# Optimization experiments

Hardware: AMD Instinct MI355X
Metric: run time of the kernel (lower is better)

Reference implementation:

```python
import jax, jax.numpy as jnp
import numpy as np

D_MODEL = 1024
NUM_HEADS = 16
HEAD_DIM = D_MODEL // NUM_HEADS


def setup_inputs() -> dict:
    key = jax.random.key(0)
    ks = jax.random.split(key, 5)
    x = jax.random.normal(ks[0], (2, 2048, D_MODEL), dtype=jnp.float32)
    # torch.nn.Linear default init ~ U(-1/sqrt(fan_in), 1/sqrt(fan_in)); scale roughly
    s = 1.0 / np.sqrt(D_MODEL)
    W_qkv = jax.random.uniform(ks[1], (D_MODEL, 3 * D_MODEL), jnp.float32, -s, s)
    b_qkv = jax.random.uniform(ks[2], (3 * D_MODEL,), jnp.float32, -s, s)
    W_out = jax.random.uniform(ks[3], (D_MODEL, D_MODEL), jnp.float32, -s, s)
    b_out = jax.random.uniform(ks[4], (D_MODEL,), jnp.float32, -s, s)
    return {"x": x, "W_qkv": W_qkv, "b_qkv": b_qkv, "W_out": W_out, "b_out": b_out}


def reference(x, W_qkv, b_qkv, W_out, b_out):
    B, S, D = x.shape
    H, Hd = NUM_HEADS, HEAD_DIM
    qkv = x @ W_qkv + b_qkv                      # [B,S,3D]
    q, k, v = jnp.split(qkv, 3, axis=-1)
    def split_heads(t):
        return t.reshape(B, S, H, Hd).transpose(0, 2, 1, 3)  # [B,H,S,Hd]
    q, k, v = split_heads(q), split_heads(k), split_heads(v)
    scores = jnp.einsum('bhqd,bhkd->bhqk', q, k) / jnp.sqrt(jnp.float32(Hd))
    weights = jax.nn.softmax(scores, axis=-1)
    attn = jnp.einsum('bhqk,bhkd->bhqd', weights, v)
    attn = attn.transpose(0, 2, 1, 3).reshape(B, S, D)
    return attn @ W_out + b_out
```

## Files before the change

kernel.cpp:

```cpp
#include <hip/hip_runtime.h>
#include <hip/hip_bf16.h>

#define DMODEL 1024
#define NH 16
#define HD 64
#define SEQ 2048
#define BATCH 2
#define BH (BATCH * NH)
#define MTOT (BATCH * SEQ)

typedef _Float16 f16x8 __attribute__((ext_vector_type(8)));
typedef _Float16 f16x4 __attribute__((ext_vector_type(4)));
typedef _Float16 f16x2 __attribute__((ext_vector_type(2)));
typedef float f32x4 __attribute__((ext_vector_type(4)));
typedef float f32x16 __attribute__((ext_vector_type(16)));

__device__ __forceinline__ void gload_lds16(const void* g, void* l) {
  __builtin_amdgcn_global_load_lds((const __attribute__((address_space(1))) unsigned*)g,
                                   (__attribute__((address_space(3))) unsigned*)l, 16, 0, 0);
}

__global__ __launch_bounds__(256) void cvt_f2h(const float* __restrict__ in,
                                               _Float16* __restrict__ out, int n8) {
  const int i = blockIdx.x * 256 + threadIdx.x;
  if (i < n8) {
    const float4 a = ((const float4*)in)[i * 2];
    const float4 b = ((const float4*)in)[i * 2 + 1];
    f16x8 o = {(_Float16)a.x, (_Float16)a.y, (_Float16)a.z, (_Float16)a.w,
               (_Float16)b.x, (_Float16)b.y, (_Float16)b.z, (_Float16)b.w};
    *(f16x8*)&out[(size_t)i * 8] = o;
  }
}

__global__ __launch_bounds__(256) void cvt_transpose(const float* __restrict__ W,
                                                     _Float16* __restrict__ Wt,
                                                     int N, int K) {
  __shared__ float Ls[64][65];
  const int k0 = blockIdx.y * 64, n0 = blockIdx.x * 64;
  const int t = threadIdx.x;
  const int r = t >> 2, c4 = (t & 3) * 16;
#pragma unroll
  for (int j = 0; j < 4; ++j) {
    const float4 v = *(const float4*)&W[(size_t)(k0 + r) * N + n0 + c4 + j * 4];
    Ls[r][c4 + j * 4 + 0] = v.x;
    Ls[r][c4 + j * 4 + 1] = v.y;
    Ls[r][c4 + j * 4 + 2] = v.z;
    Ls[r][c4 + j * 4 + 3] = v.w;
  }
  __syncthreads();
  f16x8 o0, o1;
#pragma unroll
  for (int j = 0; j < 8; ++j) {
    o0[j] = (_Float16)Ls[c4 + j][r];
    o1[j] = (_Float16)Ls[c4 + 8 + j][r];
  }
  *(f16x8*)&Wt[(size_t)(n0 + r) * K + k0 + c4] = o0;
  *(f16x8*)&Wt[(size_t)(n0 + r) * K + k0 + c4 + 8] = o1;
}

__global__ __launch_bounds__(256) void qkv_mm(const _Float16* __restrict__ A,
                                              const _Float16* __restrict__ Bt,
                                              const float* __restrict__ bias,
                                              _Float16* __restrict__ qh,
                                              _Float16* __restrict__ kh,
                                              _Float16* __restrict__ vh) {
  __shared__ __align__(16) _Float16 As[128 * 64];
  __shared__ __align__(16) _Float16 Bs[128 * 64];
  const int t = threadIdx.x;
  const int w = t >> 6, lane = t & 63;
  const int g = lane >> 4, lr = lane & 15;
  const int m0 = blockIdx.y * 128, n0 = blockIdx.x * 128;
  const int wr = w >> 1, wc = w & 1;
  const int srow = (lane >> 3);
  const int col8 = (lane & 7) * 8;
  f32x4 acc[4][4] = {};

  for (int k0 = 0; k0 < DMODEL; k0 += 64) {
    __syncthreads();
#pragma unroll
    for (int i = 0; i < 4; ++i) {
      const int row = w * 32 + i * 8 + srow;
      gload_lds16(A + (size_t)(m0 + row) * DMODEL + k0 + col8, &As[(w * 4 + i) * 512]);
      gload_lds16(Bt + (size_t)(n0 + row) * DMODEL + k0 + col8, &Bs[(w * 4 + i) * 512]);
    }
    __syncthreads();
#pragma unroll
    for (int ks = 0; ks < 2; ++ks) {
      f16x8 af[4], bf[4];
#pragma unroll
      for (int mi = 0; mi < 4; ++mi)
        af[mi] = *(const f16x8*)&As[(wr * 64 + mi * 16 + lr) * 64 + ks * 32 + g * 8];
#pragma unroll
      for (int ni = 0; ni < 4; ++ni)
        bf[ni] = *(const f16x8*)&Bs[(wc * 64 + ni * 16 + lr) * 64 + ks * 32 + g * 8];
#pragma unroll
      for (int mi = 0; mi < 4; ++mi)
#pragma unroll
        for (int ni = 0; ni < 4; ++ni)
          acc[mi][ni] = __builtin_amdgcn_mfma_f32_16x16x32_f16(af[mi], bf[ni], acc[mi][ni], 0, 0, 0);
    }
  }

#pragma unroll
  for (int ni = 0; ni < 4; ++ni) {
    const int n = n0 + wc * 64 + ni * 16 + lr;
    const float bn = bias[n];
    const int which = n >> 10, d = n & 1023, h = d >> 6, hd = d & 63;
    _Float16* dst = which == 0 ? qh : which == 1 ? kh : vh;
    const float scale = which == 0 ? 0.18033688011f : 1.0f;
#pragma unroll
    for (int mi = 0; mi < 4; ++mi)
#pragma unroll
      for (int r = 0; r < 4; ++r) {
        const int m = m0 + wr * 64 + mi * 16 + g * 4 + r;
        const int bb = m >> 11, ss = m & 2047;
        dst[((size_t)(bb * NH + h) * SEQ + ss) * HD + hd] =
            (_Float16)((acc[mi][ni][r] + bn) * scale);
      }
  }
}

__global__ __launch_bounds__(256, 2) void attn_fused(const _Float16* __restrict__ qh,
                                                     const _Float16* __restrict__ kh,
                                                     const _Float16* __restrict__ vh,
                                                     _Float16* __restrict__ ao) {
  __shared__ __align__(16) _Float16 Vt[64][76];
  const int t = threadIdx.x;
  const int lane = t & 63, w = t >> 6;
  const int q = lane & 31, hi = lane >> 5;
  const int wgid = blockIdx.x;
  const int bh = (wgid & 7) * 4 + ((wgid >> 3) & 3);
  const int qt = wgid >> 5;
  const int q0 = qt * 128 + w * 32;
  const _Float16* Qp = qh + (size_t)bh * SEQ * HD;
  const _Float16* Kp = kh + (size_t)bh * SEQ * HD;
  const _Float16* Vp = vh + (size_t)bh * SEQ * HD;

  f16x8 qf[4];
#pragma unroll
  for (int ks = 0; ks < 4; ++ks)
    qf[ks] = *(const f16x8*)(Qp + (size_t)(q0 + q) * HD + ks * 16 + hi * 8);

  f32x16 o0 = {}, o1 = {};
  float mrun = -3e30f, lrun = 0.f;

  const int skv = t & 63;
  const int sq4 = t >> 6;

  for (int kv0 = 0; kv0 < SEQ; kv0 += 64) {
    const f16x8 sv0 = *(const f16x8*)(Vp + (size_t)(kv0 + skv) * HD + sq4 * 16);
    const f16x8 sv1 = *(const f16x8*)(Vp + (size_t)(kv0 + skv) * HD + sq4 * 16 + 8);
    __syncthreads();
#pragma unroll
    for (int e = 0; e < 8; ++e) {
      Vt[sq4 * 16 + e][skv] = sv0[e];
      Vt[sq4 * 16 + 8 + e][skv] = sv1[e];
    }

    f32x16 s0 = {}, s1 = {};
    __builtin_amdgcn_s_setprio(1);
#pragma unroll
    for (int ks = 0; ks < 4; ++ks) {
      const f16x8 k0 = *(const f16x8*)(Kp + (size_t)(kv0 + q) * HD + ks * 16 + hi * 8);
      const f16x8 k1 = *(const f16x8*)(Kp + (size_t)(kv0 + 32 + q) * HD + ks * 16 + hi * 8);
      s0 = __builtin_amdgcn_mfma_f32_32x32x16_f16(k0, qf[ks], s0, 0, 0, 0);
      s1 = __builtin_amdgcn_mfma_f32_32x32x16_f16(k1, qf[ks], s1, 0, 0, 0);
    }
    __builtin_amdgcn_s_setprio(0);

    float tm[16];
#pragma unroll
    for (int r = 0; r < 16; ++r) tm[r] = fmaxf(s0[r], s1[r]);
#pragma unroll
    for (int d = 8; d > 0; d >>= 1)
#pragma unroll
      for (int r = 0; r < d; ++r) tm[r] = fmaxf(tm[r], tm[r + d]);
    const float mx = fmaxf(tm[0], __shfl_xor(tm[0], 32));
    if (!__all(mx <= mrun + 8.0f)) {
      const float mnew = fmaxf(mrun, mx);
      const float corr = exp2f(mrun - mnew);
      mrun = mnew;
      lrun *= corr;
#pragma unroll
      for (int r = 0; r < 16; ++r) {
        o0[r] *= corr;
        o1[r] *= corr;
      }
    }
#pragma unroll
    for (int r = 0; r < 16; ++r) {
      s0[r] = exp2f(s0[r] - mrun);
      s1[r] = exp2f(s1[r] - mrun);
    }
    float ts[16];
#pragma unroll
    for (int r = 0; r < 16; ++r) ts[r] = s0[r] + s1[r];
#pragma unroll
    for (int d = 8; d > 0; d >>= 1)
#pragma unroll
      for (int r = 0; r < d; ++r) ts[r] += ts[r + d];
    lrun += ts[0] + __shfl_xor(ts[0], 32);

    __syncthreads();

#pragma unroll
    for (int ks = 0; ks < 4; ++ks) {
      const int base = 8 * (ks & 1);
      unsigned u0, u1, u2, u3;
#pragma unroll
      for (int w01 = 0; w01 < 2; ++w01) {
        float a0, a1, b0, b1;
        if (ks < 2) {
          a0 = s0[base + 2 * w01];     a1 = s0[base + 2 * w01 + 1];
          b0 = s0[base + 4 + 2 * w01]; b1 = s0[base + 4 + 2 * w01 + 1];
        } else {
          a0 = s1[base + 2 * w01];     a1 = s1[base + 2 * w01 + 1];
          b0 = s1[base + 4 + 2 * w01]; b1 = s1[base + 4 + 2 * w01 + 1];
        }
        f16x2 hm0; hm0[0] = (_Float16)a0; hm0[1] = (_Float16)a1;
        f16x2 hm1; hm1[0] = (_Float16)b0; hm1[1] = (_Float16)b1;
        unsigned Pm0, Pm1;
        __builtin_memcpy(&Pm0, &hm0, 4);
        __builtin_memcpy(&Pm1, &hm1, 4);
        const unsigned local = hi ? Pm1 : Pm0;
        const unsigned sent = hi ? Pm0 : Pm1;
        const unsigned cross = __shfl_xor(sent, 32);
        const unsigned wa = hi ? cross : local;
        const unsigned wb = hi ? local : cross;
        if (w01 == 0) { u0 = wa; u2 = wb; } else { u1 = wa; u3 = wb; }
      }
      unsigned ww[4] = {u0, u1, u2, u3};
      f16x8 pb;
      __builtin_memcpy(&pb, ww, 16);
      const f16x8 va0 = *(const f16x8*)&Vt[0 + q][ks * 16 + hi * 8];
      const f16x8 va1 = *(const f16x8*)&Vt[32 + q][ks * 16 + hi * 8];
      __builtin_amdgcn_s_setprio(1);
      o0 = __builtin_amdgcn_mfma_f32_32x32x16_f16(va0, pb, o0, 0, 0, 0);
      o1 = __builtin_amdgcn_mfma_f32_32x32x16_f16(va1, pb, o1, 0, 0, 0);
      __builtin_amdgcn_s_setprio(0);
    }
  }

  const float invl = 1.0f / lrun;
  _Float16* aob = ao + (size_t)bh * SEQ * HD + (size_t)(q0 + q) * HD;
#pragma unroll
  for (int m = 0; m < 4; ++m) {
    f16x4 v0, v1;
#pragma unroll
    for (int s2 = 0; s2 < 4; ++s2) {
      v0[s2] = (_Float16)(o0[4 * m + s2] * invl);
      v1[s2] = (_Float16)(o1[4 * m + s2] * invl);
    }
    *(f16x4*)(aob + 8 * m + 4 * hi) = v0;
    *(f16x4*)(aob + 32 + 8 * m + 4 * hi) = v1;
  }
}

__global__ __launch_bounds__(256) void out_mm(const _Float16* __restrict__ Ah,
                                              const _Float16* __restrict__ Bt,
                                              const float* __restrict__ bias,
                                              float* __restrict__ out) {
  __shared__ __align__(16) _Float16 As[128 * 64];
  __shared__ __align__(16) _Float16 Bs[128 * 64];
  const int t = threadIdx.x;
  const int w = t >> 6, lane = t & 63;
  const int g = lane >> 4, lr = lane & 15;
  const int m0 = blockIdx.y * 128, n0 = blockIdx.x * 128;
  const int wr = w >> 1, wc = w & 1;
  const int srow = (lane >> 3);
  const int col8 = (lane & 7) * 8;
  f32x4 acc[4][4] = {};

  for (int k0 = 0; k0 < DMODEL; k0 += 64) {
    const int h = k0 >> 6;
    __syncthreads();
#pragma unroll
    for (int i = 0; i < 4; ++i) {
      const int row = w * 32 + i * 8 + srow;
      const int m = m0 + row;
      const int bb = m >> 11, ss = m & 2047;
      gload_lds16(Ah + ((size_t)(bb * NH + h) * SEQ + ss) * HD + col8, &As[(w * 4 + i) * 512]);
      gload_lds16(Bt + (size_t)(n0 + row) * DMODEL + k0 + col8, &Bs[(w * 4 + i) * 512]);
    }
    __syncthreads();
#pragma unroll
    for (int ks = 0; ks < 2; ++ks) {
      f16x8 af[4], bf[4];
#pragma unroll
      for (int mi = 0; mi < 4; ++mi)
        af[mi] = *(const f16x8*)&As[(wr * 64 + mi * 16 + lr) * 64 + ks * 32 + g * 8];
#pragma unroll
      for (int ni = 0; ni < 4; ++ni)
        bf[ni] = *(const f16x8*)&Bs[(wc * 64 + ni * 16 + lr) * 64 + ks * 32 + g * 8];
#pragma unroll
      for (int mi = 0; mi < 4; ++mi)
#pragma unroll
        for (int ni = 0; ni < 4; ++ni)
          acc[mi][ni] = __builtin_amdgcn_mfma_f32_16x16x32_f16(af[mi], bf[ni], acc[mi][ni], 0, 0, 0);
    }
  }

#pragma unroll
  for (int ni = 0; ni < 4; ++ni) {
    const int n = n0 + wc * 64 + ni * 16 + lr;
    const float bn = bias[n];
#pragma unroll
    for (int mi = 0; mi < 4; ++mi)
#pragma unroll
      for (int r = 0; r < 4; ++r) {
        const int m = m0 + wr * 64 + mi * 16 + g * 4 + r;
        out[(size_t)m * DMODEL + n] = acc[mi][ni][r] + bn;
      }
  }
}

extern "C" void kernel_launch(void* const* d_in, const int* in_sizes, int n_in,
                              void* d_out, int out_size, void* d_ws, size_t ws_size,
                              hipStream_t stream) {
  const float* x = (const float*)d_in[0];
  const float* Wqkv = (const float*)d_in[1];
  const float* bqkv = (const float*)d_in[2];
  const float* Wout = (const float*)d_in[3];
  const float* bout = (const float*)d_in[4];
  float* out = (float*)d_out;

  char* ws = (char*)d_ws;
  const size_t MB = 1u << 20;
  _Float16* Xh = (_Float16*)(ws);
  _Float16* qh = (_Float16*)(ws + 8 * MB);
  _Float16* kh = (_Float16*)(ws + 16 * MB);
  _Float16* vh = (_Float16*)(ws + 24 * MB);
  _Float16* Wtq = (_Float16*)(ws + 32 * MB);
  _Float16* Wto = (_Float16*)(ws + 38 * MB + 512 * 1024);
  _Float16* attnh = Xh;

  cvt_f2h<<<dim3(MTOT * DMODEL / 8 / 256), 256, 0, stream>>>(x, Xh, MTOT * DMODEL / 8);
  cvt_transpose<<<dim3(3072 / 64, DMODEL / 64), 256, 0, stream>>>(Wqkv, Wtq, 3072, DMODEL);
  cvt_transpose<<<dim3(DMODEL / 64, DMODEL / 64), 256, 0, stream>>>(Wout, Wto, DMODEL, DMODEL);
  qkv_mm<<<dim3(3072 / 128, MTOT / 128), 256, 0, stream>>>(Xh, Wtq, bqkv, qh, kh, vh);
  attn_fused<<<dim3(512), 256, 0, stream>>>(qh, kh, vh, attnh);
  out_mm<<<dim3(DMODEL / 128, MTOT / 128), 256, 0, stream>>>(attnh, Wto, bout, out);
}
```

Baseline: 259.5 us.

## Split attention KV range across two workgroups and merge with combine kernel

Attention is split along the key/value sequence into two halves, so 1024 workgroups each process half of the KV tiles. Each writes unnormalized fp32 partial outputs plus running max and sum, and a new combine kernel merges them and writes the fp16 attention output. Occupancy hint goes to 4 blocks per CU, and P conversion uses the packed cvt_pkrtz intrinsic. This adds fp32 partial-buffer traffic and an extra launch in exchange for more parallelism on 256 CUs. It falls back to the fused kernel if the workspace is too small.

```diff
diff --git a/kernel.cpp b/kernel.cpp
--- a/kernel.cpp
+++ b/kernel.cpp
@@ -11,13 +11,20 @@
 
 typedef _Float16 f16x8 __attribute__((ext_vector_type(8)));
 typedef _Float16 f16x4 __attribute__((ext_vector_type(4)));
-typedef _Float16 f16x2 __attribute__((ext_vector_type(2)));
+typedef __fp16 fp16x2 __attribute__((ext_vector_type(2)));
 typedef float f32x4 __attribute__((ext_vector_type(4)));
 typedef float f32x16 __attribute__((ext_vector_type(16)));
 
 __device__ __forceinline__ void gload_lds16(const void* g, void* l) {
   __builtin_amdgcn_global_load_lds((const __attribute__((address_space(1))) unsigned*)g,
                                    (__attribute__((address_space(3))) unsigned*)l, 16, 0, 0);
+}
+
+__device__ __forceinline__ unsigned pk16(float a, float b) {
+  const fp16x2 h = __builtin_amdgcn_cvt_pkrtz(a, b);
+  unsigned u;
+  __builtin_memcpy(&u, &h, 4);
+  return u;
 }
 
 __global__ __launch_bounds__(256) void cvt_f2h(const float* __restrict__ in,
@@ -120,6 +127,184 @@
   }
 }
 
+__device__ __forceinline__ void store_v(_Float16 (*Vt)[76], int skv, int sq4,
+                                        const f16x8& v0, const f16x8& v1) {
+#pragma unroll
+  for (int e = 0; e < 8; ++e) {
+    Vt[sq4 * 16 + e][skv] = v0[e];
+    Vt[sq4 * 16 + 8 + e][skv] = v1[e];
+  }
+}
+
+__device__ __forceinline__ void qkt_global(const _Float16* Kp, int kv0, int q, int hi,
+                                           const f16x8 (&qf)[4], f32x16& s0, f32x16& s1) {
+  s0 = {};
+  s1 = {};
+  __builtin_amdgcn_s_setprio(1);
+#pragma unroll
+  for (int ks = 0; ks < 4; ++ks) {
+    const f16x8 k0 = *(const f16x8*)(Kp + (size_t)(kv0 + q) * HD + ks * 16 + hi * 8);
+    const f16x8 k1 = *(const f16x8*)(Kp + (size_t)(kv0 + 32 + q) * HD + ks * 16 + hi * 8);
+    s0 = __builtin_amdgcn_mfma_f32_32x32x16_f16(k0, qf[ks], s0, 0, 0, 0);
+    s1 = __builtin_amdgcn_mfma_f32_32x32x16_f16(k1, qf[ks], s1, 0, 0, 0);
+  }
+  __builtin_amdgcn_s_setprio(0);
+}
+
+__device__ __forceinline__ void softmax_update(f32x16& s0, f32x16& s1, float& mrun,
+                                               float& lrun, f32x16& o0, f32x16& o1) {
+  float tm[16];
+#pragma unroll
+  for (int r = 0; r < 16; ++r) tm[r] = fmaxf(s0[r], s1[r]);
+#pragma unroll
+  for (int d = 8; d > 0; d >>= 1)
+#pragma unroll
+    for (int r = 0; r < d; ++r) tm[r] = fmaxf(tm[r], tm[r + d]);
+  const float mx = fmaxf(tm[0], __shfl_xor(tm[0], 32));
+  if (!__all(mx <= mrun + 8.0f)) {
+    const float mnew = fmaxf(mrun, mx);
+    const float corr = exp2f(mrun - mnew);
+    mrun = mnew;
+    lrun *= corr;
+#pragma unroll
+    for (int r = 0; r < 16; ++r) {
+      o0[r] *= corr;
+      o1[r] *= corr;
+    }
+  }
+#pragma unroll
+  for (int r = 0; r < 16; ++r) {
+    s0[r] = exp2f(s0[r] - mrun);
+    s1[r] = exp2f(s1[r] - mrun);
+  }
+  float ts[16];
+#pragma unroll
+  for (int r = 0; r < 16; ++r) ts[r] = s0[r] + s1[r];
+#pragma unroll
+  for (int d = 8; d > 0; d >>= 1)
+#pragma unroll
+    for (int r = 0; r < d; ++r) ts[r] += ts[r + d];
+  lrun += ts[0] + __shfl_xor(ts[0], 32);
+}
+
+__device__ __forceinline__ void pv(const f32x16& s0, const f32x16& s1,
+                                   const _Float16 (*Vt)[76], int q, int hi,
+                                   f32x16& o0, f32x16& o1) {
+#pragma unroll
+  for (int ks = 0; ks < 4; ++ks) {
+    const int base = 8 * (ks & 1);
+    unsigned u0, u1, u2, u3;
+#pragma unroll
+    for (int w01 = 0; w01 < 2; ++w01) {
+      float a0, a1, b0, b1;
+      if (ks < 2) {
+        a0 = s0[base + 2 * w01];     a1 = s0[base + 2 * w01 + 1];
+        b0 = s0[base + 4 + 2 * w01]; b1 = s0[base + 4 + 2 * w01 + 1];
+      } else {
+        a0 = s1[base + 2 * w01];     a1 = s1[base + 2 * w01 + 1];
+        b0 = s1[base + 4 + 2 * w01]; b1 = s1[base + 4 + 2 * w01 + 1];
+      }
+      const unsigned Pm0 = pk16(a0, a1);
+      const unsigned Pm1 = pk16(b0, b1);
+      const unsigned local = hi ? Pm1 : Pm0;
+      const unsigned sent = hi ? Pm0 : Pm1;
+      const unsigned cross = __shfl_xor(sent, 32);
+      const unsigned wa = hi ? cross : local;
+      const unsigned wb = hi ? local : cross;
+      if (w01 == 0) { u0 = wa; u2 = wb; } else { u1 = wa; u3 = wb; }
+    }
+    unsigned ww[4] = {u0, u1, u2, u3};
+    f16x8 pb;
+    __builtin_memcpy(&pb, ww, 16);
+    const f16x8 va0 = *(const f16x8*)&Vt[0 + q][ks * 16 + hi * 8];
+    const f16x8 va1 = *(const f16x8*)&Vt[32 + q][ks * 16 + hi * 8];
+    __builtin_amdgcn_s_setprio(1);
+    o0 = __builtin_amdgcn_mfma_f32_32x32x16_f16(va0, pb, o0, 0, 0, 0);
+    o1 = __builtin_amdgcn_mfma_f32_32x32x16_f16(va1, pb, o1, 0, 0, 0);
+    __builtin_amdgcn_s_setprio(0);
+  }
+}
+
+__global__ __launch_bounds__(256, 4) void attn_part(const _Float16* __restrict__ qh,
+                                                    const _Float16* __restrict__ kh,
+                                                    const _Float16* __restrict__ vh,
+                                                    float* __restrict__ Op,
+                                                    float* __restrict__ ml) {
+  __shared__ __align__(16) _Float16 Vt[64][76];
+  const int t = threadIdx.x;
+  const int lane = t & 63, w = t >> 6;
+  const int q = lane & 31, hi = lane >> 5;
+  const int wgid = blockIdx.x;
+  const int bh = (wgid & 7) * 4 + ((wgid >> 3) & 3);
+  const int rest = wgid >> 5;
+  const int qt = rest & 15, half = rest >> 4;
+  const int q0 = qt * 128 + w * 32;
+  const int kvlo = half * (SEQ / 2);
+  const _Float16* Qp = qh + (size_t)bh * SEQ * HD;
+  const _Float16* Kp = kh + (size_t)bh * SEQ * HD;
+  const _Float16* Vp = vh + (size_t)bh * SEQ * HD;
+
+  f16x8 qf[4];
+#pragma unroll
+  for (int ks = 0; ks < 4; ++ks)
+    qf[ks] = *(const f16x8*)(Qp + (size_t)(q0 + q) * HD + ks * 16 + hi * 8);
+
+  f32x16 o0 = {}, o1 = {};
+  float mrun = -3e30f, lrun = 0.f;
+  const int skv = t & 63;
+  const int sq4 = t >> 6;
+
+  for (int kv0 = kvlo; kv0 < kvlo + SEQ / 2; kv0 += 64) {
+    const f16x8 sv0 = *(const f16x8*)(Vp + (size_t)(kv0 + skv) * HD + sq4 * 16);
+    const f16x8 sv1 = *(const f16x8*)(Vp + (size_t)(kv0 + skv) * HD + sq4 * 16 + 8);
+    __syncthreads();
+    store_v(Vt, skv, sq4, sv0, sv1);
+    f32x16 s0, s1;
+    qkt_global(Kp, kv0, q, hi, qf, s0, s1);
+    softmax_update(s0, s1, mrun, lrun, o0, o1);
+    __syncthreads();
+    pv(s0, s1, Vt, q, hi, o0, o1);
+  }
+
+  const size_t row = (size_t)bh * SEQ + q0 + q;
+  float* Ob = Op + ((size_t)half * BH * SEQ + row) * HD;
+#pragma unroll
+  for (int m = 0; m < 4; ++m) {
+    f32x4 a = {o0[4 * m + 0], o0[4 * m + 1], o0[4 * m + 2], o0[4 * m + 3]};
+    f32x4 b = {o1[4 * m + 0], o1[4 * m + 1], o1[4 * m + 2], o1[4 * m + 3]};
+    *(f32x4*)(Ob + 8 * m + 4 * hi) = a;
+    *(f32x4*)(Ob + 32 + 8 * m + 4 * hi) = b;
+  }
+  if (hi == 0) {
+    ml[((size_t)half * BH * SEQ + row) * 2 + 0] = mrun;
+    ml[((size_t)half * BH * SEQ + row) * 2 + 1] = lrun;
+  }
+}
+
+__global__ __launch_bounds__(256) void attn_combine(const float* __restrict__ Op,
+                                                    const float* __restrict__ ml,
+                                                    _Float16* __restrict__ ao) {
+  const int tid = blockIdx.x * 256 + threadIdx.x;
+  const size_t row = tid >> 3;
+  const int dblk = (tid & 7) * 8;
+  const float* A = Op + row * HD + dblk;
+  const float* B = Op + (size_t)BH * SEQ * HD + row * HD + dblk;
+  const float ma = ml[row * 2], la = ml[row * 2 + 1];
+  const float mb = ml[((size_t)BH * SEQ + row) * 2], lb = ml[((size_t)BH * SEQ + row) * 2 + 1];
+  const float m = fmaxf(ma, mb);
+  const float fa = exp2f(ma - m), fb = exp2f(mb - m);
+  const float inv = 1.0f / (la * fa + lb * fb);
+  const f32x4 a0 = *(const f32x4*)A, a1 = *(const f32x4*)(A + 4);
+  const f32x4 b0 = *(const f32x4*)B, b1 = *(const f32x4*)(B + 4);
+  f16x8 o;
+#pragma unroll
+  for (int j = 0; j < 4; ++j) {
+    o[j] = (_Float16)((a0[j] * fa + b0[j] * fb) * inv);
+    o[4 + j] = (_Float16)((a1[j] * fa + b1[j] * fb) * inv);
+  }
+  *(f16x8*)(ao + row * HD + dblk) = o;
+}
+
 __global__ __launch_bounds__(256, 2) void attn_fused(const _Float16* __restrict__ qh,
                                                      const _Float16* __restrict__ kh,
                                                      const _Float16* __restrict__ vh,
@@ -143,7 +328,6 @@
 
   f32x16 o0 = {}, o1 = {};
   float mrun = -3e30f, lrun = 0.f;
-
   const int skv = t & 63;
   const int sq4 = t >> 6;
 
@@ -151,94 +335,12 @@
     const f16x8 sv0 = *(const f16x8*)(Vp + (size_t)(kv0 + skv) * HD + sq4 * 16);
     const f16x8 sv1 = *(const f16x8*)(Vp + (size_t)(kv0 + skv) * HD + sq4 * 16 + 8);
     __syncthreads();
-#pragma unroll
-    for (int e = 0; e < 8; ++e) {
-      Vt[sq4 * 16 + e][skv] = sv0[e];
-      Vt[sq4 * 16 + 8 + e][skv] = sv1[e];
-    }
-
-    f32x16 s0 = {}, s1 = {};
-    __builtin_amdgcn_s_setprio(1);
-#pragma unroll
-    for (int ks = 0; ks < 4; ++ks) {
-      const f16x8 k0 = *(const f16x8*)(Kp + (size_t)(kv0 + q) * HD + ks * 16 + hi * 8);
-      const f16x8 k1 = *(const f16x8*)(Kp + (size_t)(kv0 + 32 + q) * HD + ks * 16 + hi * 8);
-      s0 = __builtin_amdgcn_mfma_f32_32x32x16_f16(k0, qf[ks], s0, 0, 0, 0);
-      s1 = __builtin_amdgcn_mfma_f32_32x32x16_f16(k1, qf[ks], s1, 0, 0, 0);
-    }
-    __builtin_amdgcn_s_setprio(0);
-
-    float tm[16];
-#pragma unroll
-    for (int r = 0; r < 16; ++r) tm[r] = fmaxf(s0[r], s1[r]);
-#pragma unroll
-    for (int d = 8; d > 0; d >>= 1)
-#pragma unroll
-      for (int r = 0; r < d; ++r) tm[r] = fmaxf(tm[r], tm[r + d]);
-    const float mx = fmaxf(tm[0], __shfl_xor(tm[0], 32));
-    if (!__all(mx <= mrun + 8.0f)) {
-      const float mnew = fmaxf(mrun, mx);
-      const float corr = exp2f(mrun - mnew);
-      mrun = mnew;
-      lrun *= corr;
-#pragma unroll
-      for (int r = 0; r < 16; ++r) {
-        o0[r] *= corr;
-        o1[r] *= corr;
-      }
-    }
-#pragma unroll
-    for (int r = 0; r < 16; ++r) {
-      s0[r] = exp2f(s0[r] - mrun);
-      s1[r] = exp2f(s1[r] - mrun);
-    }
-    float ts[16];
-#pragma unroll
-    for (int r = 0; r < 16; ++r) ts[r] = s0[r] + s1[r];
-#pragma unroll
-    for (int d = 8; d > 0; d >>= 1)
-#pragma unroll
-      for (int r = 0; r < d; ++r) ts[r] += ts[r + d];
-    lrun += ts[0] + __shfl_xor(ts[0], 32);
-
-    __syncthreads();
-
-#pragma unroll
-    for (int ks = 0; ks < 4; ++ks) {
-      const int base = 8 * (ks & 1);
-      unsigned u0, u1, u2, u3;
-#pragma unroll
-      for (int w01 = 0; w01 < 2; ++w01) {
-        float a0, a1, b0, b1;
-        if (ks < 2) {
-          a0 = s0[base + 2 * w01];     a1 = s0[base + 2 * w01 + 1];
-          b0 = s0[base + 4 + 2 * w01]; b1 = s0[base + 4 + 2 * w01 + 1];
-        } else {
-          a0 = s1[base + 2 * w01];     a1 = s1[base + 2 * w01 + 1];
-          b0 = s1[base + 4 + 2 * w01]; b1 = s1[base + 4 + 2 * w01 + 1];
-        }
-        f16x2 hm0; hm0[0] = (_Float16)a0; hm0[1] = (_Float16)a1;
-        f16x2 hm1; hm1[0] = (_Float16)b0; hm1[1] = (_Float16)b1;
-        unsigned Pm0, Pm1;
-        __builtin_memcpy(&Pm0, &hm0, 4);
-        __builtin_memcpy(&Pm1, &hm1, 4);
-        const unsigned local = hi ? Pm1 : Pm0;
-        const unsigned sent = hi ? Pm0 : Pm1;
-        const unsigned cross = __shfl_xor(sent, 32);
-        const unsigned wa = hi ? cross : local;
-        const unsigned wb = hi ? local : cross;
-        if (w01 == 0) { u0 = wa; u2 = wb; } else { u1 = wa; u3 = wb; }
-      }
-      unsigned ww[4] = {u0, u1, u2, u3};
-      f16x8 pb;
-      __builtin_memcpy(&pb, ww, 16);
-      const f16x8 va0 = *(const f16x8*)&Vt[0 + q][ks * 16 + hi * 8];
-      const f16x8 va1 = *(const f16x8*)&Vt[32 + q][ks * 16 + hi * 8];
-      __builtin_amdgcn_s_setprio(1);
-      o0 = __builtin_amdgcn_mfma_f32_32x32x16_f16(va0, pb, o0, 0, 0, 0);
-      o1 = __builtin_amdgcn_mfma_f32_32x32x16_f16(va1, pb, o1, 0, 0, 0);
-      __builtin_amdgcn_s_setprio(0);
-    }
+    store_v(Vt, skv, sq4, sv0, sv1);
+    f32x16 s0, s1;
+    qkt_global(Kp, kv0, q, hi, qf, s0, s1);
+    softmax_update(s0, s1, mrun, lrun, o0, o1);
+    __syncthreads();
+    pv(s0, s1, Vt, q, hi, o0, o1);
   }
 
   const float invl = 1.0f / lrun;
@@ -334,10 +436,20 @@
   _Float16* Wto = (_Float16*)(ws + 38 * MB + 512 * 1024);
   _Float16* attnh = Xh;
 
+  float* Op = (float*)(ws + 48 * MB);
+  float* mlp = (float*)(ws + 48 * MB + (size_t)2 * BH * SEQ * HD * 4);
+  const size_t ws_needed = 48 * MB + (size_t)2 * BH * SEQ * HD * 4 +
+                           (size_t)2 * BH * SEQ * 2 * 4;
+
   cvt_f2h<<<dim3(MTOT * DMODEL / 8 / 256), 256, 0, stream>>>(x, Xh, MTOT * DMODEL / 8);
   cvt_transpose<<<dim3(3072 / 64, DMODEL / 64), 256, 0, stream>>>(Wqkv, Wtq, 3072, DMODEL);
   cvt_transpose<<<dim3(DMODEL / 64, DMODEL / 64), 256, 0, stream>>>(Wout, Wto, DMODEL, DMODEL);
   qkv_mm<<<dim3(3072 / 128, MTOT / 128), 256, 0, stream>>>(Xh, Wtq, bqkv, qh, kh, vh);
-  attn_fused<<<dim3(512), 256, 0, stream>>>(qh, kh, vh, attnh);
+  if (ws_size >= ws_needed) {
+    attn_part<<<dim3(1024), 256, 0, stream>>>(qh, kh, vh, Op, mlp);
+    attn_combine<<<dim3(BH * SEQ * 8 / 256), 256, 0, stream>>>(Op, mlp, attnh);
+  } else {
+    attn_fused<<<dim3(512), 256, 0, stream>>>(qh, kh, vh, attnh);
+  }
   out_mm<<<dim3(DMODEL / 128, MTOT / 128), 256, 0, stream>>>(attnh, Wto, bout, out);
 }
```

Result: slower. 273.6 us (+5.4%).
